# Kernel optimization log

Hardware: AMD Instinct MI355X
Metric: run time of the kernel (lower is better)

The kernel has to match this reference:

```python
import jax, jax.numpy as jnp
import numpy as np

D_K = 64  # hardcoded in source module

def setup_inputs() -> dict:
    key = jax.random.key(0)
    kq, kk, kv, km = jax.random.split(key, 4)
    B, H, S, D = 2, 16, 2048, D_K
    Q = jax.random.normal(kq, (B, H, S, D), dtype=jnp.float32)
    K = jax.random.normal(kk, (B, H, S, D), dtype=jnp.float32)
    V = jax.random.normal(kv, (B, H, S, D), dtype=jnp.float32)
    # boolean mask: True positions are masked out (filled with -1e9)
    attn_mask = jax.random.randint(km, (B, H, S, S), 0, 2) == 1
    return {"Q": Q, "K": K, "V": V, "attn_mask": attn_mask}

def reference(Q, K, V, attn_mask):
    scale = 1.0 / np.sqrt(D_K).astype(np.float32)
    # scores: [B, H, S, S]
    scores = jnp.einsum('bhqd,bhkd->bhqk', Q, K) * scale
    scores = jnp.where(attn_mask, jnp.float32(-1e9), scores)
    attn = jax.nn.softmax(scores, axis=-1)
    context = jnp.einsum('bhqk,bhkd->bhqd', attn, V)
    return context
```

## Files before the change

kernel.cpp:

```cpp
#include <hip/hip_runtime.h>

#define SEQ   2048
#define DK    64
#define QBLK  64
#define KVBLK 32
#define NWAVE 4

typedef __attribute__((ext_vector_type(8))) __bf16 bf16x8;
typedef __attribute__((ext_vector_type(4))) float  f32x4;

__device__ __forceinline__ float grp16_max(float v) {
  v = fmaxf(v, __shfl_xor(v, 1));
  v = fmaxf(v, __shfl_xor(v, 2));
  v = fmaxf(v, __shfl_xor(v, 4));
  v = fmaxf(v, __shfl_xor(v, 8));
  return v;
}
__device__ __forceinline__ float grp16_sum(float v) {
  v += __shfl_xor(v, 1);
  v += __shfl_xor(v, 2);
  v += __shfl_xor(v, 4);
  v += __shfl_xor(v, 8);
  return v;
}

__global__ __launch_bounds__(256, 4)
void sdpa_fwd(const float* __restrict__ Q, const float* __restrict__ K,
              const float* __restrict__ V, const int* __restrict__ M,
              float* __restrict__ O)
{
  __shared__ __bf16 Klds[KVBLK][72];
  __shared__ __bf16 Vt[DK][40];
  __shared__ __bf16 Plds[NWAVE][16][40];

  const int tid  = threadIdx.x;
  const int w    = tid >> 6;
  const int lane = tid & 63;
  const int g    = lane >> 4;
  const int li   = lane & 15;

  const int blk = blockIdx.x;
  const int qb  = blk & (SEQ / QBLK - 1);
  const int bh  = blk >> 5;

  const float* Qp = Q + (size_t)bh * SEQ * DK;
  const float* Kp = K + (size_t)bh * SEQ * DK;
  const float* Vp = V + (size_t)bh * SEQ * DK;
  const int*   Mp = M + (size_t)bh * SEQ * SEQ;
  float*       Op = O + (size_t)bh * SEQ * DK;

  const int q0 = qb * QBLK + w * 16;

  bf16x8 qfrag[2];
  {
    const float qs = 0.125f * 1.44269504088896340736f;
    const float* qr = Qp + (size_t)(q0 + li) * DK + g * 8;
    #pragma unroll
    for (int h2 = 0; h2 < 2; ++h2) {
      f32x4 a = *(const f32x4*)(qr + h2 * 32);
      f32x4 b = *(const f32x4*)(qr + h2 * 32 + 4);
      bf16x8 f;
      #pragma unroll
      for (int e = 0; e < 4; ++e) {
        f[e]     = (__bf16)(a[e] * qs);
        f[4 + e] = (__bf16)(b[e] * qs);
      }
      qfrag[h2] = f;
    }
  }

  f32x4 acc[4];
  #pragma unroll
  for (int c = 0; c < 4; ++c) acc[c] = (f32x4){0.f, 0.f, 0.f, 0.f};
  float m_r[4], l_r[4];
  #pragma unroll
  for (int r = 0; r < 4; ++r) { m_r[r] = -__builtin_inff(); l_r[r] = 0.f; }

  for (int kt = 0; kt < SEQ / KVBLK; ++kt) {
    const int kv0 = kt * KVBLK;
    __syncthreads();

    {
      const int row = tid >> 3;
      const int col = (tid & 7) * 8;
      const float* ks = Kp + (size_t)(kv0 + row) * DK + col;
      f32x4 a = *(const f32x4*)ks;
      f32x4 b = *(const f32x4*)(ks + 4);
      bf16x8 kb;
      #pragma unroll
      for (int e = 0; e < 4; ++e) { kb[e] = (__bf16)a[e]; kb[4 + e] = (__bf16)b[e]; }
      *(bf16x8*)&Klds[row][col] = kb;

      const float* vs = Vp + (size_t)(kv0 + row) * DK + col;
      f32x4 va = *(const f32x4*)vs;
      f32x4 vb = *(const f32x4*)(vs + 4);
      #pragma unroll
      for (int e = 0; e < 4; ++e) {
        Vt[col + e][row]     = (__bf16)va[e];
        Vt[col + 4 + e][row] = (__bf16)vb[e];
      }
    }
    __syncthreads();

    f32x4 st[2];
    #pragma unroll
    for (int t2 = 0; t2 < 2; ++t2) {
      bf16x8 k0 = *(const bf16x8*)&Klds[t2 * 16 + li][g * 8];
      bf16x8 k1 = *(const bf16x8*)&Klds[t2 * 16 + li][32 + g * 8];
      f32x4 s = (f32x4){0.f, 0.f, 0.f, 0.f};
      s = __builtin_amdgcn_mfma_f32_16x16x32_bf16(qfrag[0], k0, s, 0, 0, 0);
      s = __builtin_amdgcn_mfma_f32_16x16x32_bf16(qfrag[1], k1, s, 0, 0, 0);
      st[t2] = s;
    }

    #pragma unroll
    for (int r = 0; r < 4; ++r) {
      const size_t mrow = (size_t)(q0 + 4 * g + r) * SEQ + kv0;
      float s0 = st[0][r];
      float s1 = st[1][r];
      if (Mp[mrow + li])      s0 = -1e9f;
      if (Mp[mrow + 16 + li]) s1 = -1e9f;
      float mx    = grp16_max(fmaxf(s0, s1));
      float mnew  = fmaxf(m_r[r], mx);
      float alpha = __builtin_amdgcn_exp2f(m_r[r] - mnew);
      float p0    = __builtin_amdgcn_exp2f(s0 - mnew);
      float p1    = __builtin_amdgcn_exp2f(s1 - mnew);
      l_r[r] = l_r[r] * alpha + grp16_sum(p0 + p1);
      m_r[r] = mnew;
      acc[0][r] *= alpha;
      acc[1][r] *= alpha;
      acc[2][r] *= alpha;
      acc[3][r] *= alpha;
      Plds[w][4 * g + r][li]      = (__bf16)p0;
      Plds[w][4 * g + r][16 + li] = (__bf16)p1;
    }

    asm volatile("s_waitcnt lgkmcnt(0)" ::: "memory");
    __builtin_amdgcn_sched_barrier(0);

    bf16x8 pf = *(const bf16x8*)&Plds[w][li][g * 8];
    #pragma unroll
    for (int c = 0; c < 4; ++c) {
      bf16x8 vf = *(const bf16x8*)&Vt[c * 16 + li][g * 8];
      acc[c] = __builtin_amdgcn_mfma_f32_16x16x32_bf16(pf, vf, acc[c], 0, 0, 0);
    }
  }

  #pragma unroll
  for (int r = 0; r < 4; ++r) {
    float inv = 1.0f / l_r[r];
    float* orow = Op + (size_t)(q0 + 4 * g + r) * DK + li;
    orow[0]  = acc[0][r] * inv;
    orow[16] = acc[1][r] * inv;
    orow[32] = acc[2][r] * inv;
    orow[48] = acc[3][r] * inv;
  }
}

extern "C" void kernel_launch(void* const* d_in, const int* in_sizes, int n_in,
                              void* d_out, int out_size, void* d_ws, size_t ws_size,
                              hipStream_t stream) {
  const float* Q = (const float*)d_in[0];
  const float* K = (const float*)d_in[1];
  const float* V = (const float*)d_in[2];
  const int*   M = (const int*)d_in[3];
  float*       O = (float*)d_out;

  const int nblocks = 2 * 16 * (SEQ / QBLK);
  sdpa_fwd<<<nblocks, 256, 0, stream>>>(Q, K, V, M, O);
}
```

Before: 818.4 us.

## Double KV tile to 64, prefetch next tile and vectorize mask loads

Enlarges the KV tile to 64 keys and register-prefetches the next tile's K, V and mask while the current tile computes. Keys are permuted within the tile so that each lane's four score columns map to four consecutive mask ints, which allows a single 16-byte mask load per row instead of scalar loads. It aims to hide global latency on the dominant mask stream and to halve barrier count. The cost is higher register pressure, with occupancy hint lowered to 2.

```diff
diff --git a/kernel.cpp b/kernel.cpp
--- a/kernel.cpp
+++ b/kernel.cpp
@@ -3,11 +3,14 @@
 #define SEQ   2048
 #define DK    64
 #define QBLK  64
-#define KVBLK 32
-#define NWAVE 4
+#define KVBLK 64
+#define NTILE (SEQ / KVBLK)
+#define PITCH 72
 
 typedef __attribute__((ext_vector_type(8))) __bf16 bf16x8;
+typedef __attribute__((ext_vector_type(4))) __bf16 bf16x4;
 typedef __attribute__((ext_vector_type(4))) float  f32x4;
+typedef __attribute__((ext_vector_type(4))) int    i32x4;
 
 __device__ __forceinline__ float grp16_max(float v) {
   v = fmaxf(v, __shfl_xor(v, 1));
@@ -24,14 +27,14 @@
   return v;
 }
 
-__global__ __launch_bounds__(256, 4)
+__global__ __launch_bounds__(256, 2)
 void sdpa_fwd(const float* __restrict__ Q, const float* __restrict__ K,
               const float* __restrict__ V, const int* __restrict__ M,
               float* __restrict__ O)
 {
-  __shared__ __bf16 Klds[KVBLK][72];
-  __shared__ __bf16 Vt[DK][40];
-  __shared__ __bf16 Plds[NWAVE][16][40];
+  __shared__ __bf16 Klds[KVBLK][PITCH];
+  __shared__ __bf16 Vt[DK][PITCH];
+  __shared__ __bf16 Plds[4][16][PITCH];
 
   const int tid  = threadIdx.x;
   const int w    = tid >> 6;
@@ -50,6 +53,10 @@
   float*       Op = O + (size_t)bh * SEQ * DK;
 
   const int q0 = qb * QBLK + w * 16;
+
+  const int sk = tid >> 2;
+  const int sd = (tid & 3) * 16;
+  const int sj = ((sk & 3) << 4) | (sk >> 2);
 
   bf16x8 qfrag[2];
   {
@@ -76,73 +83,103 @@
   #pragma unroll
   for (int r = 0; r < 4; ++r) { m_r[r] = -__builtin_inff(); l_r[r] = 0.f; }
 
-  for (int kt = 0; kt < SEQ / KVBLK; ++kt) {
-    const int kv0 = kt * KVBLK;
+  f32x4 kA[4], vA[4];
+  i32x4 mA[4];
+
+  {
+    const float* ks = Kp + (size_t)sk * DK + sd;
+    const float* vs = Vp + (size_t)sk * DK + sd;
+    #pragma unroll
+    for (int i = 0; i < 4; ++i) { kA[i] = *(const f32x4*)(ks + 4 * i); vA[i] = *(const f32x4*)(vs + 4 * i); }
+    #pragma unroll
+    for (int r = 0; r < 4; ++r)
+      mA[r] = *(const i32x4*)(Mp + (size_t)(q0 + 4 * g + r) * SEQ + li * 4);
+  }
+
+  for (int kt = 0; kt < NTILE; ++kt) {
     __syncthreads();
 
     {
-      const int row = tid >> 3;
-      const int col = (tid & 7) * 8;
-      const float* ks = Kp + (size_t)(kv0 + row) * DK + col;
-      f32x4 a = *(const f32x4*)ks;
-      f32x4 b = *(const f32x4*)(ks + 4);
-      bf16x8 kb;
-      #pragma unroll
-      for (int e = 0; e < 4; ++e) { kb[e] = (__bf16)a[e]; kb[4 + e] = (__bf16)b[e]; }
-      *(bf16x8*)&Klds[row][col] = kb;
-
-      const float* vs = Vp + (size_t)(kv0 + row) * DK + col;
-      f32x4 va = *(const f32x4*)vs;
-      f32x4 vb = *(const f32x4*)(vs + 4);
+      bf16x8 klo, khi;
       #pragma unroll
       for (int e = 0; e < 4; ++e) {
-        Vt[col + e][row]     = (__bf16)va[e];
-        Vt[col + 4 + e][row] = (__bf16)vb[e];
+        klo[e]     = (__bf16)kA[0][e];
+        klo[4 + e] = (__bf16)kA[1][e];
+        khi[e]     = (__bf16)kA[2][e];
+        khi[4 + e] = (__bf16)kA[3][e];
       }
-    }
+      *(bf16x8*)&Klds[sj][sd]     = klo;
+      *(bf16x8*)&Klds[sj][sd + 8] = khi;
+      #pragma unroll
+      for (int qd = 0; qd < 4; ++qd)
+        #pragma unroll
+        for (int e = 0; e < 4; ++e)
+          Vt[sd + qd * 4 + e][sk] = (__bf16)vA[qd][e];
+    }
+
+    i32x4 msk[4];
+    #pragma unroll
+    for (int r = 0; r < 4; ++r) msk[r] = mA[r];
+
+    if (kt + 1 < NTILE) {
+      const int kvn = (kt + 1) * KVBLK;
+      const float* ks = Kp + (size_t)(kvn + sk) * DK + sd;
+      const float* vs = Vp + (size_t)(kvn + sk) * DK + sd;
+      #pragma unroll
+      for (int i = 0; i < 4; ++i) { kA[i] = *(const f32x4*)(ks + 4 * i); vA[i] = *(const f32x4*)(vs + 4 * i); }
+      #pragma unroll
+      for (int r = 0; r < 4; ++r)
+        mA[r] = *(const i32x4*)(Mp + (size_t)(q0 + 4 * g + r) * SEQ + kvn + li * 4);
+    }
+
     __syncthreads();
 
-    f32x4 st[2];
-    #pragma unroll
-    for (int t2 = 0; t2 < 2; ++t2) {
-      bf16x8 k0 = *(const bf16x8*)&Klds[t2 * 16 + li][g * 8];
-      bf16x8 k1 = *(const bf16x8*)&Klds[t2 * 16 + li][32 + g * 8];
+    f32x4 st[4];
+    #pragma unroll
+    for (int nt = 0; nt < 4; ++nt) {
+      bf16x8 b0 = *(const bf16x8*)&Klds[nt * 16 + li][g * 8];
+      bf16x8 b1 = *(const bf16x8*)&Klds[nt * 16 + li][32 + g * 8];
       f32x4 s = (f32x4){0.f, 0.f, 0.f, 0.f};
-      s = __builtin_amdgcn_mfma_f32_16x16x32_bf16(qfrag[0], k0, s, 0, 0, 0);
-      s = __builtin_amdgcn_mfma_f32_16x16x32_bf16(qfrag[1], k1, s, 0, 0, 0);
-      st[t2] = s;
+      s = __builtin_amdgcn_mfma_f32_16x16x32_bf16(qfrag[0], b0, s, 0, 0, 0);
+      s = __builtin_amdgcn_mfma_f32_16x16x32_bf16(qfrag[1], b1, s, 0, 0, 0);
+      st[nt] = s;
     }
 
     #pragma unroll
     for (int r = 0; r < 4; ++r) {
-      const size_t mrow = (size_t)(q0 + 4 * g + r) * SEQ + kv0;
-      float s0 = st[0][r];
-      float s1 = st[1][r];
-      if (Mp[mrow + li])      s0 = -1e9f;
-      if (Mp[mrow + 16 + li]) s1 = -1e9f;
-      float mx    = grp16_max(fmaxf(s0, s1));
+      float s0 = msk[r].x ? -1e9f : st[0][r];
+      float s1 = msk[r].y ? -1e9f : st[1][r];
+      float s2 = msk[r].z ? -1e9f : st[2][r];
+      float s3 = msk[r].w ? -1e9f : st[3][r];
+      float mx    = grp16_max(fmaxf(fmaxf(s0, s1), fmaxf(s2, s3)));
       float mnew  = fmaxf(m_r[r], mx);
       float alpha = __builtin_amdgcn_exp2f(m_r[r] - mnew);
-      float p0    = __builtin_amdgcn_exp2f(s0 - mnew);
-      float p1    = __builtin_amdgcn_exp2f(s1 - mnew);
-      l_r[r] = l_r[r] * alpha + grp16_sum(p0 + p1);
+      float p0 = __builtin_amdgcn_exp2f(s0 - mnew);
+      float p1 = __builtin_amdgcn_exp2f(s1 - mnew);
+      float p2 = __builtin_amdgcn_exp2f(s2 - mnew);
+      float p3 = __builtin_amdgcn_exp2f(s3 - mnew);
+      l_r[r] = l_r[r] * alpha + grp16_sum((p0 + p1) + (p2 + p3));
       m_r[r] = mnew;
       acc[0][r] *= alpha;
       acc[1][r] *= alpha;
       acc[2][r] *= alpha;
       acc[3][r] *= alpha;
-      Plds[w][4 * g + r][li]      = (__bf16)p0;
-      Plds[w][4 * g + r][16 + li] = (__bf16)p1;
+      bf16x4 pk;
+      pk[0] = (__bf16)p0; pk[1] = (__bf16)p1; pk[2] = (__bf16)p2; pk[3] = (__bf16)p3;
+      *(bf16x4*)&Plds[w][4 * g + r][li * 4] = pk;
     }
 
     asm volatile("s_waitcnt lgkmcnt(0)" ::: "memory");
     __builtin_amdgcn_sched_barrier(0);
 
-    bf16x8 pf = *(const bf16x8*)&Plds[w][li][g * 8];
-    #pragma unroll
-    for (int c = 0; c < 4; ++c) {
-      bf16x8 vf = *(const bf16x8*)&Vt[c * 16 + li][g * 8];
-      acc[c] = __builtin_amdgcn_mfma_f32_16x16x32_bf16(pf, vf, acc[c], 0, 0, 0);
+    bf16x8 pa0 = *(const bf16x8*)&Plds[w][li][g * 8];
+    bf16x8 pa1 = *(const bf16x8*)&Plds[w][li][32 + g * 8];
+    #pragma unroll
+    for (int dt = 0; dt < 4; ++dt) {
+      bf16x8 v0 = *(const bf16x8*)&Vt[dt * 16 + li][g * 8];
+      bf16x8 v1 = *(const bf16x8*)&Vt[dt * 16 + li][32 + g * 8];
+      acc[dt] = __builtin_amdgcn_mfma_f32_16x16x32_bf16(pa0, v0, acc[dt], 0, 0, 0);
+      acc[dt] = __builtin_amdgcn_mfma_f32_16x16x32_bf16(pa1, v1, acc[dt], 0, 0, 0);
     }
   }
 
@@ -150,10 +187,9 @@
   for (int r = 0; r < 4; ++r) {
     float inv = 1.0f / l_r[r];
     float* orow = Op + (size_t)(q0 + 4 * g + r) * DK + li;
-    orow[0]  = acc[0][r] * inv;
-    orow[16] = acc[1][r] * inv;
-    orow[32] = acc[2][r] * inv;
-    orow[48] = acc[3][r] * inv;
+    #pragma unroll
+    for (int dt = 0; dt < 4; ++dt)
+      orow[dt * 16] = acc[dt][r] * inv;
   }
 }
 
```

After: 753.9 us. 1.09x faster.
